# Optimization experiments

Hardware: AMD Instinct MI355X
Metric: run time of the kernel (lower is better)

Reference implementation:

```python
import jax, jax.numpy as jnp
import numpy as np

B, V, E, L, D = 16, 19, 361, 256, 64  # batch, vertices, edges/graph, seq_len, d_model
F_IN = 2 * D + 1  # concat(src_feat, tgt_feat, edge_weight)


def _linear_init(key, fan_in, fan_out):
    bound = 1.0 / np.sqrt(fan_in)
    kw, kb = jax.random.split(key)
    W = jax.random.uniform(kw, (fan_in, fan_out), jnp.float32, -bound, bound)
    b = jax.random.uniform(kb, (fan_out,), jnp.float32, -bound, bound)
    return W, b


def setup_inputs() -> dict:
    key = jax.random.key(0)
    ks = jax.random.split(key, 6)
    hidden_states = jax.random.normal(ks[0], (B * V, L, D), jnp.float32)
    edge_index = jax.random.randint(ks[1], (2, B * E, L), 0, B * V, dtype=jnp.int32)
    edge_weight = jax.random.uniform(ks[2], (B * E, L), jnp.float32)
    W1, b1 = _linear_init(ks[3], F_IN, D)
    W2, b2 = _linear_init(ks[4], D, D // 2)
    W3, b3 = _linear_init(ks[5], D // 2, 1)
    skip_param = jnp.float32(0.25)
    return {"hidden_states": hidden_states, "edge_weight": edge_weight,
            "W1": W1, "b1": b1, "W2": W2, "b2": b2, "W3": W3, "b3": b3,
            "skip_param": skip_param, "edge_index": edge_index}


def reference(hidden_states, edge_weight, W1, b1, W2, b2, W3, b3, skip_param, edge_index):
    # hidden_states: (B*V, L, D) -> (B, L, V, D) for per-timestep node gather
    hs = hidden_states.reshape(B, V, L, D).transpose(0, 2, 1, 3)
    # edge indices are global node ids; local vertex id = idx % V (as in torch code)
    src = (edge_index[0] % V).reshape(B, E, L).transpose(0, 2, 1)  # (B, L, E)
    tgt = (edge_index[1] % V).reshape(B, E, L).transpose(0, 2, 1)
    ew = edge_weight.reshape(B, E, L).transpose(0, 2, 1)           # (B, L, E)
    src_feat = jnp.take_along_axis(hs, src[..., None], axis=2)    # (B, L, E, D)
    tgt_feat = jnp.take_along_axis(hs, tgt[..., None], axis=2)    # (B, L, E, D)
    x = jnp.concatenate([src_feat, tgt_feat, ew[..., None]], axis=-1)  # (B, L, E, 2D+1)
    h = jax.nn.silu(x @ W1 + b1)
    h = jax.nn.silu(h @ W2 + b2)
    w = jax.nn.sigmoid((h @ W3 + b3)[..., 0])                     # (B, L, E)
    new_ew = skip_param * ew + (1.0 - skip_param) * w
    return new_ew.transpose(0, 2, 1).reshape(B * E, L)            # (B*E, L)
```

## Files before the change

kernel.cpp:

```cpp
#include <hip/hip_runtime.h>

#define NB 16
#define NV 19
#define NE 361
#define NL 256
#define ND 64
#define NTW 23
#define NEPW (NTW * 16)
#define ASTRIDE 136

typedef __attribute__((ext_vector_type(8))) short bf16x8;
typedef __attribute__((ext_vector_type(4))) float f32x4;
typedef __attribute__((ext_vector_type(2))) __bf16 bf16v2;

union bf8u { unsigned u[4]; bf16x8 v; uint4 q; };

__device__ __forceinline__ unsigned pack_bf16(float lo, float hi) {
    bf16v2 v; v.x = (__bf16)lo; v.y = (__bf16)hi;
    return __builtin_bit_cast(unsigned, v);
}
__device__ __forceinline__ short f2bf(float f) {
    __bf16 h = (__bf16)f;
    return __builtin_bit_cast(short, h);
}
__device__ __forceinline__ float bflo(unsigned u) {
    return __builtin_bit_cast(float, u << 16);
}
__device__ __forceinline__ float bfhi(unsigned u) {
    return __builtin_bit_cast(float, u & 0xffff0000u);
}
__device__ __forceinline__ f32x4 silu4(f32x4 x) {
    f32x4 t = x * -1.44269504f;
    f32x4 d;
    d.x = __builtin_amdgcn_exp2f(t.x);
    d.y = __builtin_amdgcn_exp2f(t.y);
    d.z = __builtin_amdgcn_exp2f(t.z);
    d.w = __builtin_amdgcn_exp2f(t.w);
    d += 1.f;
    f32x4 r;
    r.x = __builtin_amdgcn_rcpf(d.x);
    r.y = __builtin_amdgcn_rcpf(d.y);
    r.z = __builtin_amdgcn_rcpf(d.z);
    r.w = __builtin_amdgcn_rcpf(d.w);
    return x * r;
}
__device__ __forceinline__ float sigm(float x) {
    return __builtin_amdgcn_rcpf(1.f + __builtin_amdgcn_exp2f(x * -1.44269504f));
}

__global__ __launch_bounds__(256, 4) void edge_learner_kernel(
    const float* __restrict__ hs,
    const float* __restrict__ ew_in,
    const float* __restrict__ W1,
    const float* __restrict__ b1,
    const float* __restrict__ W2,
    const float* __restrict__ b2,
    const float* __restrict__ W3,
    const float* __restrict__ b3,
    const float* __restrict__ skip_p,
    const int*   __restrict__ eidx,
    float* __restrict__ out)
{
    __shared__ __align__(16) short A_s[4][NV * ASTRIDE];
    __shared__ __align__(8)  uint2 meta_s[4][NEPW];

    const int tid  = threadIdx.x;
    const int lane = tid & 63;
    const int wave = tid >> 6;
    const int lq   = lane >> 4;
    const int lm   = lane & 15;
    const int bid0 = blockIdx.x;
    const int bid  = (bid0 & 7) * 128 + (bid0 >> 3);
    const int pairid = bid * 4 + wave;
    const int b    = pairid >> 8;
    const int l    = pairid & 255;

    short*  Aw = A_s[wave];
    uint2*  Mw = meta_s[wave];

    for (int e = lane; e < NEPW; e += 64) {
        uint2 m;
        if (e < NE) {
            size_t row = (size_t)(b * NE + e) * NL + l;
            unsigned so = (unsigned)((eidx[row] % NV) * ASTRIDE);
            unsigned to = (unsigned)((eidx[(size_t)NB * NE * NL + row] % NV) * ASTRIDE + 64);
            m.x = so | (to << 16);
            m.y = __builtin_bit_cast(unsigned, ew_in[row]);
        } else {
            m.x = 64u << 16; m.y = 0u;
        }
        Mw[e] = m;
    }

    f32x4 w1lv[2][2];
    #pragma unroll
    for (int ks = 0; ks < 2; ++ks) {
        w1lv[ks][0] = *(const f32x4*)&W1[128 * 64 + ks * 32 + lq * 8];
        w1lv[ks][1] = *(const f32x4*)&W1[128 * 64 + ks * 32 + lq * 8 + 4];
    }
    bf8u w2f[2][2];
    #pragma unroll
    for (int nt = 0; nt < 2; ++nt)
        #pragma unroll
        for (int ks = 0; ks < 2; ++ks) {
            const float* w2p = &W2[(ks * 32 + lq * 8) * 32 + nt * 16 + lm];
            #pragma unroll
            for (int p = 0; p < 4; ++p)
                w2f[nt][ks].u[p] = pack_bf16(w2p[(2 * p) * 32], w2p[(2 * p + 1) * 32]);
        }
    const f32x4 b2v0 = *(const f32x4*)&b2[lq * 4];
    const f32x4 b2v1 = *(const f32x4*)&b2[16 + lq * 4];
    const f32x4 w3v0 = *(const f32x4*)&W3[lq * 4];
    const f32x4 w3v1 = *(const f32x4*)&W3[16 + lq * 4];
    const float b3v  = b3[0];
    const float skip = skip_p[0];

    {
        bf8u af[2][2];
        #pragma unroll
        for (int Mt = 0; Mt < 2; ++Mt) {
            int v  = Mt * 16 + lm;
            int vc = v < NV ? v : NV - 1;
            const float* hp = hs + ((size_t)(b * NV + vc) * NL + l) * ND;
            #pragma unroll
            for (int ks = 0; ks < 2; ++ks) {
                float4 x0 = *(const float4*)&hp[ks * 32 + lq * 8];
                float4 x1 = *(const float4*)&hp[ks * 32 + lq * 8 + 4];
                af[Mt][ks].u[0] = pack_bf16(x0.x, x0.y);
                af[Mt][ks].u[1] = pack_bf16(x0.z, x0.w);
                af[Mt][ks].u[2] = pack_bf16(x1.x, x1.y);
                af[Mt][ks].u[3] = pack_bf16(x1.z, x1.w);
            }
        }
        #pragma unroll
        for (int cg = 0; cg < 4; ++cg) {
            const int half = cg >> 1;
            const int oc0  = (cg & 1) * 32;
            const float hb0 = 0.5f * b1[(cg * 32 + lm) & 63];
            const float hb1 = 0.5f * b1[(cg * 32 + 16 + lm) & 63];
            bf8u w1f[2][2];
            #pragma unroll
            for (int nt = 0; nt < 2; ++nt)
                #pragma unroll
                for (int ks = 0; ks < 2; ++ks) {
                    const float* wp = &W1[(half * 64 + ks * 32 + lq * 8) * 64
                                          + oc0 + nt * 16 + lm];
                    #pragma unroll
                    for (int p = 0; p < 4; ++p)
                        w1f[nt][ks].u[p] = pack_bf16(wp[(2 * p) * 64], wp[(2 * p + 1) * 64]);
                }
            f32x4 a00 = {0,0,0,0}, a01 = {0,0,0,0}, a10 = {0,0,0,0}, a11 = {0,0,0,0};
            a00 = __builtin_amdgcn_mfma_f32_16x16x32_bf16(af[0][0].v, w1f[0][0].v, a00, 0, 0, 0);
            a00 = __builtin_amdgcn_mfma_f32_16x16x32_bf16(af[0][1].v, w1f[0][1].v, a00, 0, 0, 0);
            a01 = __builtin_amdgcn_mfma_f32_16x16x32_bf16(af[0][0].v, w1f[1][0].v, a01, 0, 0, 0);
            a01 = __builtin_amdgcn_mfma_f32_16x16x32_bf16(af[0][1].v, w1f[1][1].v, a01, 0, 0, 0);
            a10 = __builtin_amdgcn_mfma_f32_16x16x32_bf16(af[1][0].v, w1f[0][0].v, a10, 0, 0, 0);
            a10 = __builtin_amdgcn_mfma_f32_16x16x32_bf16(af[1][1].v, w1f[0][1].v, a10, 0, 0, 0);
            a11 = __builtin_amdgcn_mfma_f32_16x16x32_bf16(af[1][0].v, w1f[1][0].v, a11, 0, 0, 0);
            a11 = __builtin_amdgcn_mfma_f32_16x16x32_bf16(af[1][1].v, w1f[1][1].v, a11, 0, 0, 0);
            #pragma unroll
            for (int r = 0; r < 4; ++r) {
                int v0 = lq * 4 + r;
                Aw[v0 * ASTRIDE + cg * 32 + lm]      = f2bf(a00[r] + hb0);
                Aw[v0 * ASTRIDE + cg * 32 + 16 + lm] = f2bf(a01[r] + hb1);
                int v1 = 16 + lq * 4 + r;
                if (v1 < NV) {
                    Aw[v1 * ASTRIDE + cg * 32 + lm]      = f2bf(a10[r] + hb0);
                    Aw[v1 * ASTRIDE + cg * 32 + 16 + lm] = f2bf(a11[r] + hb1);
                }
            }
        }
    }

    for (int t = 0; t < NTW; ++t) {
        const uint2 m = Mw[t * 16 + lm];
        const int so = (int)(m.x & 0xffffu);
        const int to = (int)(m.x >> 16);
        const float ew = __builtin_bit_cast(float, m.y);

        bf8u a1[2];
        #pragma unroll
        for (int ks = 0; ks < 2; ++ks) {
            const uint4 as = *(const uint4*)&Aw[so + ks * 32 + lq * 8];
            const uint4 at = *(const uint4*)&Aw[to + ks * 32 + lq * 8];
            f32x4 x0, x1;
            x0.x = bflo(as.x) + bflo(at.x);
            x0.y = bfhi(as.x) + bfhi(at.x);
            x0.z = bflo(as.y) + bflo(at.y);
            x0.w = bfhi(as.y) + bfhi(at.y);
            x1.x = bflo(as.z) + bflo(at.z);
            x1.y = bfhi(as.z) + bfhi(at.z);
            x1.z = bflo(as.w) + bflo(at.w);
            x1.w = bfhi(as.w) + bfhi(at.w);
            x0 += ew * w1lv[ks][0];
            x1 += ew * w1lv[ks][1];
            f32x4 y0 = silu4(x0);
            f32x4 y1 = silu4(x1);
            a1[ks].u[0] = pack_bf16(y0.x, y0.y);
            a1[ks].u[1] = pack_bf16(y0.z, y0.w);
            a1[ks].u[2] = pack_bf16(y1.x, y1.y);
            a1[ks].u[3] = pack_bf16(y1.z, y1.w);
        }

        f32x4 c0 = {0,0,0,0}, c1 = {0,0,0,0};
        c0 = __builtin_amdgcn_mfma_f32_16x16x32_bf16(w2f[0][0].v, a1[0].v, c0, 0, 0, 0);
        c0 = __builtin_amdgcn_mfma_f32_16x16x32_bf16(w2f[0][1].v, a1[1].v, c0, 0, 0, 0);
        c1 = __builtin_amdgcn_mfma_f32_16x16x32_bf16(w2f[1][0].v, a1[0].v, c1, 0, 0, 0);
        c1 = __builtin_amdgcn_mfma_f32_16x16x32_bf16(w2f[1][1].v, a1[1].v, c1, 0, 0, 0);

        f32x4 h0 = silu4(c0 + b2v0);
        f32x4 h1 = silu4(c1 + b2v1);
        f32x4 pv = h0 * w3v0 + h1 * w3v1;
        float p  = (pv.x + pv.y) + (pv.z + pv.w);
        p += __shfl_xor(p, 16);
        p += __shfl_xor(p, 32);

        if (lane < 16) {
            int er = t * 16 + lane;
            if (er < NE) {
                float wgt = sigm(p + b3v);
                out[(size_t)(b * NE + er) * NL + l] = skip * ew + (1.f - skip) * wgt;
            }
        }
    }
}

extern "C" void kernel_launch(void* const* d_in, const int* in_sizes, int n_in,
                              void* d_out, int out_size, void* d_ws, size_t ws_size,
                              hipStream_t stream) {
    const float* hs   = (const float*)d_in[0];
    const float* ew   = (const float*)d_in[1];
    const float* W1   = (const float*)d_in[2];
    const float* b1   = (const float*)d_in[3];
    const float* W2   = (const float*)d_in[4];
    const float* b2   = (const float*)d_in[5];
    const float* W3   = (const float*)d_in[6];
    const float* b3   = (const float*)d_in[7];
    const float* skip = (const float*)d_in[8];
    const int*   eidx = (const int*)d_in[9];
    float* outp = (float*)d_out;

    dim3 grid(NB * NL / 4);
    dim3 block(256);
    hipLaunchKernelGGL(edge_learner_kernel, grid, block, 0, stream,
                       hs, ew, W1, b1, W2, b2, W3, b3, skip, eidx, outp);
}
```

Measured before the change: 68.55 us.

## Launch one single-wave block per (batch, timestep) pair instead of four-wave blocks

Each block now holds one 64-thread wave handling a single (b,l) pair, with its own LDS tile and metadata, replacing 256-thread blocks that packed four independent waves. The grid grows fourfold and the block-index swizzle is adjusted to match. Because the waves never shared data, this should let the scheduler place and retire waves independently and avoid holding a block's resources until its slowest wave finishes. The cost is more blocks to dispatch, and the launch-bounds hint changes, which may alter register allocation.

```diff
diff --git a/kernel.cpp b/kernel.cpp
--- a/kernel.cpp
+++ b/kernel.cpp
@@ -48,7 +48,7 @@
     return __builtin_amdgcn_rcpf(1.f + __builtin_amdgcn_exp2f(x * -1.44269504f));
 }
 
-__global__ __launch_bounds__(256, 4) void edge_learner_kernel(
+__global__ __launch_bounds__(64, 7) void edge_learner_kernel(
     const float* __restrict__ hs,
     const float* __restrict__ ew_in,
     const float* __restrict__ W1,
@@ -61,22 +61,16 @@
     const int*   __restrict__ eidx,
     float* __restrict__ out)
 {
-    __shared__ __align__(16) short A_s[4][NV * ASTRIDE];
-    __shared__ __align__(8)  uint2 meta_s[4][NEPW];
-
-    const int tid  = threadIdx.x;
-    const int lane = tid & 63;
-    const int wave = tid >> 6;
+    __shared__ __align__(16) short A_s[NV * ASTRIDE];
+    __shared__ __align__(8)  uint2 meta_s[NEPW];
+
+    const int lane = threadIdx.x;
     const int lq   = lane >> 4;
     const int lm   = lane & 15;
     const int bid0 = blockIdx.x;
-    const int bid  = (bid0 & 7) * 128 + (bid0 >> 3);
-    const int pairid = bid * 4 + wave;
-    const int b    = pairid >> 8;
-    const int l    = pairid & 255;
-
-    short*  Aw = A_s[wave];
-    uint2*  Mw = meta_s[wave];
+    const int bid  = (bid0 & 7) * 512 + (bid0 >> 3);
+    const int b    = bid >> 8;
+    const int l    = bid & 255;
 
     for (int e = lane; e < NEPW; e += 64) {
         uint2 m;
@@ -89,7 +83,7 @@
         } else {
             m.x = 64u << 16; m.y = 0u;
         }
-        Mw[e] = m;
+        meta_s[e] = m;
     }
 
     f32x4 w1lv[2][2];
@@ -161,19 +155,19 @@
             #pragma unroll
             for (int r = 0; r < 4; ++r) {
                 int v0 = lq * 4 + r;
-                Aw[v0 * ASTRIDE + cg * 32 + lm]      = f2bf(a00[r] + hb0);
-                Aw[v0 * ASTRIDE + cg * 32 + 16 + lm] = f2bf(a01[r] + hb1);
+                A_s[v0 * ASTRIDE + cg * 32 + lm]      = f2bf(a00[r] + hb0);
+                A_s[v0 * ASTRIDE + cg * 32 + 16 + lm] = f2bf(a01[r] + hb1);
                 int v1 = 16 + lq * 4 + r;
                 if (v1 < NV) {
-                    Aw[v1 * ASTRIDE + cg * 32 + lm]      = f2bf(a10[r] + hb0);
-                    Aw[v1 * ASTRIDE + cg * 32 + 16 + lm] = f2bf(a11[r] + hb1);
+                    A_s[v1 * ASTRIDE + cg * 32 + lm]      = f2bf(a10[r] + hb0);
+                    A_s[v1 * ASTRIDE + cg * 32 + 16 + lm] = f2bf(a11[r] + hb1);
                 }
             }
         }
     }
 
     for (int t = 0; t < NTW; ++t) {
-        const uint2 m = Mw[t * 16 + lm];
+        const uint2 m = meta_s[t * 16 + lm];
         const int so = (int)(m.x & 0xffffu);
         const int to = (int)(m.x >> 16);
         const float ew = __builtin_bit_cast(float, m.y);
@@ -181,8 +175,8 @@
         bf8u a1[2];
         #pragma unroll
         for (int ks = 0; ks < 2; ++ks) {
-            const uint4 as = *(const uint4*)&Aw[so + ks * 32 + lq * 8];
-            const uint4 at = *(const uint4*)&Aw[to + ks * 32 + lq * 8];
+            const uint4 as = *(const uint4*)&A_s[so + ks * 32 + lq * 8];
+            const uint4 at = *(const uint4*)&A_s[to + ks * 32 + lq * 8];
             f32x4 x0, x1;
             x0.x = bflo(as.x) + bflo(at.x);
             x0.y = bfhi(as.x) + bfhi(at.x);
@@ -240,8 +234,8 @@
     const int*   eidx = (const int*)d_in[9];
     float* outp = (float*)d_out;
 
-    dim3 grid(NB * NL / 4);
-    dim3 block(256);
+    dim3 grid(NB * NL);
+    dim3 block(64);
     hipLaunchKernelGGL(edge_learner_kernel, grid, block, 0, stream,
                        hs, ew, W1, b1, W2, b2, W3, b3, skip, eidx, outp);
 }
```

After: 68.99 us. No clear change (+0.7%).
